# Performance work log

Measured on AMD Instinct MI355X. Metric: run time of the kernel, lower is better.

Reference implementation:

```python
import jax, jax.numpy as jnp
import numpy as np

B, P, T, V, H, E, C = 256, 256, 32, 3433, 512, 300, 128


def _gru(x, h, W_ih, W_hh, b_ih, b_hh):
    # torch.nn.GRUCell math (bias=True default)
    gx = x @ W_ih.T + b_ih          # (B, 3H)
    gh = h @ W_hh.T + b_hh          # (B, 3H)
    xr, xz, xn = jnp.split(gx, 3, axis=-1)
    hr, hz, hn = jnp.split(gh, 3, axis=-1)
    r = jax.nn.sigmoid(xr + hr)
    z = jax.nn.sigmoid(xz + hz)
    n = jnp.tanh(xn + r * hn)
    return (1.0 - z) * n + z * h


def setup_inputs() -> dict:
    key = jax.random.key(0)
    ks = jax.random.split(key, 24)
    s = 0.02
    inp = {
        'word_embs': jax.random.normal(ks[0], (B, T, E), jnp.float32),
        't_feat': jax.random.normal(ks[1], (B, C), jnp.float32),
        'c_feats': jax.random.normal(ks[2], (B, P, C), jnp.float32),
        'num_words': T,
        # top-down unit (all Linears bias=False)
        'W_td1': jax.random.normal(ks[3], (128, H), jnp.float32) * s,
        'W_td2': jax.random.normal(ks[4], (128, C), jnp.float32) * s,
        'W_td3': jax.random.normal(ks[5], (128, E), jnp.float32) * s,
        'W_td':  jax.random.normal(ks[6], (128, 128), jnp.float32) * s,
        'W1_ih': jax.random.normal(ks[7], (3 * H, 128), jnp.float32) * s,
        'W1_hh': jax.random.normal(ks[8], (3 * H, H), jnp.float32) * s,
        'b1_ih': jax.random.normal(ks[9], (3 * H,), jnp.float32) * s,
        'b1_hh': jax.random.normal(ks[10], (3 * H,), jnp.float32) * s,
        # additive attention
        'W_feat': jax.random.normal(ks[11], (H, C), jnp.float32) * s,
        'W_hidd': jax.random.normal(ks[12], (H, H), jnp.float32) * s,
        'W_att':  jax.random.normal(ks[13], (1, H), jnp.float32) * s,
        # language unit
        'W_l1': jax.random.normal(ks[14], (128, C), jnp.float32) * s,
        'W_l2': jax.random.normal(ks[15], (128, H), jnp.float32) * s,
        'W_l':  jax.random.normal(ks[16], (128, 128), jnp.float32) * s,
        'W2_ih': jax.random.normal(ks[17], (3 * H, 128), jnp.float32) * s,
        'W2_hh': jax.random.normal(ks[18], (3 * H, H), jnp.float32) * s,
        'b2_ih': jax.random.normal(ks[19], (3 * H,), jnp.float32) * s,
        'b2_hh': jax.random.normal(ks[20], (3 * H,), jnp.float32) * s,
        # classifier (bias=True)
        'W_cls': jax.random.normal(ks[21], (V, H), jnp.float32) * s,
        'b_cls': jax.random.normal(ks[22], (V,), jnp.float32) * s,
    }
    return inp


def reference(word_embs, t_feat, c_feats, num_words,
              W_td1, W_td2, W_td3, W_td, W1_ih, W1_hh, b1_ih, b1_hh,
              W_feat, W_hidd, W_att, W_l1, W_l2, W_l,
              W2_ih, W2_hh, b2_ih, b2_hh, W_cls, b_cls):
    n_steps = num_words - 1  # python int, static
    # precompute attention key projection of proposals: (B, P, H)
    feat_proj = jnp.einsum('bpc,hc->bph', c_feats, W_feat)
    td_t = t_feat @ W_td2.T  # (B, 128), time-invariant

    def step_fn(carry, x_t):
        h1, h2 = carry
        # top-down input
        s = x_t @ W_td3.T + h2 @ W_td1.T + td_t
        s = jax.nn.relu(jnp.tanh(s) @ W_td.T)
        h1 = _gru(s, h1, W1_ih, W1_hh, b1_ih, b1_hh)
        # additive attention over proposals
        comb = jnp.tanh(feat_proj + (h1 @ W_hidd.T)[:, None, :])  # (B, P, H)
        scores = jnp.einsum('bph,h->bp', comb, W_att[0])           # (B, P)
        mask = jax.nn.softmax(scores, axis=1)                      # (B, P)
        attended = jnp.einsum('bpc,bp->bc', c_feats, mask)         # (B, C)
        # language input
        l = jnp.tanh(attended @ W_l1.T + h1 @ W_l2.T)
        l = jax.nn.relu(l @ W_l.T)
        h2 = _gru(l, h2, W2_ih, W2_hh, b2_ih, b2_hh)
        logits = h2 @ W_cls.T + b_cls                              # (B, V)
        return (h1, h2), (logits, mask)

    h0 = (jnp.zeros((word_embs.shape[0], H), word_embs.dtype),
          jnp.zeros((word_embs.shape[0], H), word_embs.dtype))
    xs = jnp.swapaxes(word_embs[:, :n_steps], 0, 1)  # (T-1, B, E)
    _, (logits, masks) = jax.lax.scan(step_fn, h0, xs)
    lang_cap = jnp.swapaxes(logits, 0, 1)            # (B, T-1, V)
    topdown_attn = jnp.transpose(masks, (1, 2, 0))   # (B, P, T-1)
    return lang_cap, topdown_attn
```

## Files before the change

kernel.cpp:

```cpp
#include <hip/hip_runtime.h>
#include <hip/hip_bf16.h>

namespace {

constexpr int kB  = 256;
constexpr int kP  = 256;
constexpr int kT  = 32;
constexpr int kNS = 31;
constexpr int kV  = 3433;
constexpr int kH  = 512;
constexpr int kE  = 300;
constexpr int kC  = 128;
constexpr int kG  = 1536;
constexpr int kLdsStride = 40;

typedef __bf16 bf16x8 __attribute__((ext_vector_type(8)));
typedef float f32x4 __attribute__((ext_vector_type(4)));

__device__ __forceinline__ float fexp2(float x) {
  float r; asm("v_exp_f32 %0, %1" : "=v"(r) : "v"(x)); return r;
}
__device__ __forceinline__ float frcp(float x) {
  float r; asm("v_rcp_f32 %0, %1" : "=v"(r) : "v"(x)); return r;
}
__device__ __forceinline__ float ftanh(float x) {
  float e = fexp2(x * 2.8853900817779268f);
  return 1.0f - 2.0f * frcp(e + 1.0f);
}
__device__ __forceinline__ float fsigm(float x) {
  return frcp(1.0f + fexp2(x * -1.4426950408889634f));
}
__device__ __forceinline__ unsigned short f2bf(float f) {
  unsigned u = __float_as_uint(f);
  u += 0x7FFFu + ((u >> 16) & 1u);
  return (unsigned short)(u >> 16);
}
__device__ __forceinline__ float bf2f(unsigned short s) {
  return __uint_as_float((unsigned)s << 16);
}
__device__ __forceinline__ bf16x8 bload(const unsigned short* p) {
  union { uint4 u; bf16x8 v; } x;
  x.u = *(const uint4*)p;
  return x.v;
}

__global__ void k_transpose(const float* s0, const float* s1, const float* s2,
                            const float* s3, const float* s4, const float* s5,
                            const float* s6, const float* s7, const float* s8,
                            float* d0, float* d1, float* d2, float* d3,
                            float* d4, float* d5, float* d6, float* d7,
                            float* d8) {
  const float* src; float* dst; int R, Cd;
  switch (blockIdx.y) {
    case 0:  src = s0; dst = d0; R = 128;  Cd = 300; break;
    case 1:  src = s1; dst = d1; R = 128;  Cd = 512; break;
    case 2:  src = s2; dst = d2; R = 128;  Cd = 128; break;
    case 3:  src = s3; dst = d3; R = 128;  Cd = 128; break;
    case 4:  src = s4; dst = d4; R = 128;  Cd = 512; break;
    case 5:  src = s5; dst = d5; R = 128;  Cd = 128; break;
    case 6:  src = s6; dst = d6; R = 1536; Cd = 128; break;
    case 7:  src = s7; dst = d7; R = 1536; Cd = 128; break;
    default: src = s8; dst = d8; R = 512;  Cd = 512; break;
  }
  int n = R * Cd;
  for (int i = blockIdx.x * blockDim.x + threadIdx.x; i < n;
       i += gridDim.x * blockDim.x) {
    int k = i / R, r = i - k * R;
    dst[i] = src[r * Cd + k];
  }
}

__global__ void k_tobf16(const float* s0, const float* s1, const float* s2,
                         const float* s3, const float* s4, const float* s5,
                         const float* s6, const float* s7,
                         unsigned short* d0, unsigned short* d1,
                         unsigned short* d2, unsigned short* d3,
                         unsigned short* d4, unsigned short* d5,
                         unsigned short* d6, unsigned short* d7) {
  const float* s; unsigned short* d; int n;
  switch (blockIdx.y) {
    case 0:  s = s0; d = d0; n = kC * kC; break;
    case 1:  s = s1; d = d1; n = kH * kC; break;
    case 2:  s = s2; d = d2; n = kC * kC; break;
    case 3:  s = s3; d = d3; n = kC * kG; break;
    case 4:  s = s4; d = d4; n = kH * kH; break;
    case 5:  s = s5; d = d5; n = kH * kC; break;
    case 6:  s = s6; d = d6; n = kC * kC; break;
    default: s = s7; d = d7; n = kC * kG; break;
  }
  for (int i = blockIdx.x * blockDim.x + threadIdx.x; i < n;
       i += gridDim.x * blockDim.x)
    d[i] = f2bf(s[i]);
}

__global__ void k_split(const float* s0, const float* s1, const float* s2,
                        const float* s3,
                        unsigned short* h0, unsigned short* l0,
                        unsigned short* h1, unsigned short* l1,
                        unsigned short* h2, unsigned short* l2,
                        unsigned short* h3, unsigned short* l3) {
  const float* s; unsigned short* h; unsigned short* l; int n;
  switch (blockIdx.y) {
    case 0:  s = s0; h = h0; l = l0; n = kG * kH; break;
    case 1:  s = s1; h = h1; l = l1; n = kG * kH; break;
    case 2:  s = s2; h = h2; l = l2; n = kV * kH; break;
    default: s = s3; h = h3; l = l3; n = kH * kC; break;
  }
  for (int i = blockIdx.x * blockDim.x + threadIdx.x; i < n;
       i += gridDim.x * blockDim.x) {
    float v = s[i];
    unsigned short hb = f2bf(v);
    h[i] = hb;
    l[i] = f2bf(v - bf2f(hb));
  }
}

__global__ void k_init(const float* __restrict__ t_feat,
                       const float* __restrict__ W_td2,
                       float* __restrict__ td, float* __restrict__ h1,
                       float* __restrict__ h2,
                       unsigned short* __restrict__ h1h,
                       unsigned short* __restrict__ h1l,
                       unsigned short* __restrict__ h2h,
                       unsigned short* __restrict__ h2l) {
  int tid = blockIdx.x * 256 + threadIdx.x;
  int b = tid >> 7, c = tid & 127;
  const float* tf = t_feat + b * kC;
  const float* w  = W_td2 + c * kC;
  float acc = 0.f;
  for (int k = 0; k < kC; ++k) acc = fmaf(tf[k], w[k], acc);
  td[tid] = acc;
  for (int i = tid; i < kB * kH; i += (1 << 15)) {
    h1[i] = 0.f; h2[i] = 0.f;
    h1h[i] = 0; h1l[i] = 0; h2h[i] = 0; h2l[i] = 0;
  }
}

__global__ __launch_bounds__(256) void k_xw(
    const float* __restrict__ word_embs, const float* __restrict__ td3t,
    const float* __restrict__ td, float* __restrict__ xw) {
  __shared__ float xl[4 * 300];
  __shared__ float tdl[512];
  int t = blockIdx.y, b0 = blockIdx.x * 4, tid = threadIdx.x;
  #pragma unroll
  for (int r = 0; r < 4; ++r) {
    const float* xs = word_embs + (size_t)(b0 + r) * (kT * kE) + (size_t)t * kE;
    for (int e = tid; e < kE; e += 256) xl[r * kE + e] = xs[e];
  }
  for (int i = tid; i < 512; i += 256) tdl[i] = td[(size_t)b0 * kC + i];
  __syncthreads();
  #pragma unroll
  for (int q = 0; q < 2; ++q) {
    int idx = tid + q * 256;
    int r = idx >> 7, c = idx & 127;
    float acc = tdl[idx];
    const float* xr = xl + r * kE;
    const float* w3 = td3t + c;
    for (int e = 0; e < kE; ++e) acc = fmaf(xr[e], w3[(size_t)e * 128], acc);
    xw[((size_t)t * kB + b0 + r) * kC + c] = acc;
  }
}

__global__ __launch_bounds__(256) void k_prestep(
    const float* __restrict__ xw, const unsigned short* __restrict__ tdbt,
    const unsigned short* __restrict__ iht1b, const float* __restrict__ b1_ih,
    float* __restrict__ gx1) {
  __shared__ float s1l[128];
  __shared__ float s2l[128];
  __shared__ float part[256];
  int b = blockIdx.x, tid = threadIdx.x;
  if (tid < 128) s1l[tid] = ftanh(xw[(size_t)b * kC + tid]);
  __syncthreads();
  {
    int c = tid & 127, g = tid >> 7;
    float s = 0.f;
    const unsigned short* w = tdbt + (size_t)(g * 64) * kC + c;
    for (int k = 0; k < 64; ++k)
      s = fmaf(s1l[g * 64 + k], bf2f(w[(size_t)k * kC]), s);
    part[g * 128 + c] = s;
  }
  __syncthreads();
  if (tid < 128) s2l[tid] = fmaxf(part[tid] + part[128 + tid], 0.f);
  __syncthreads();
  #pragma unroll
  for (int q = 0; q < 6; ++q) {
    int j = q * 256 + tid;
    float acc = b1_ih[j];
    const unsigned short* w = iht1b + j;
    for (int k = 0; k < kC; ++k)
      acc = fmaf(s2l[k], bf2f(w[(size_t)k * kG]), acc);
    gx1[(size_t)b * kG + j] = acc;
  }
}

__device__ __forceinline__ void mm_tile_lds(
    const unsigned short* __restrict__ Ah, const unsigned short* __restrict__ Al,
    const unsigned short* __restrict__ Bh, const unsigned short* __restrict__ Bl,
    int m0, int n0, int K, int kbeg, int kend, int nMax, f32x4 acc[4][4],
    unsigned short* sAh, unsigned short* sAl,
    unsigned short* sBh, unsigned short* sBl) {
  int tid = threadIdx.x;
  int lane = tid & 63, wid = tid >> 6;
  int wm = (wid >> 1) * 64, wn = (wid & 1) * 64;
  int r16 = lane & 15, kq = lane >> 4;
  int rA = tid >> 2, cA = (tid & 3) * 8;
  int brow0 = n0 + rA;       if (brow0 > nMax) brow0 = nMax;
  int brow1 = n0 + rA + 64;  if (brow1 > nMax) brow1 = nMax;
  for (int k0 = kbeg; k0 < kend; k0 += 32) {
    uint4 va0 = *(const uint4*)(Ah + (size_t)(m0 + rA) * K + k0 + cA);
    uint4 va1 = *(const uint4*)(Ah + (size_t)(m0 + rA + 64) * K + k0 + cA);
    uint4 vb0 = *(const uint4*)(Al + (size_t)(m0 + rA) * K + k0 + cA);
    uint4 vb1 = *(const uint4*)(Al + (size_t)(m0 + rA + 64) * K + k0 + cA);
    uint4 vc0 = *(const uint4*)(Bh + (size_t)brow0 * K + k0 + cA);
    uint4 vc1 = *(const uint4*)(Bh + (size_t)brow1 * K + k0 + cA);
    uint4 vd0 = *(const uint4*)(Bl + (size_t)brow0 * K + k0 + cA);
    uint4 vd1 = *(const uint4*)(Bl + (size_t)brow1 * K + k0 + cA);
    __syncthreads();
    *(uint4*)&sAh[rA * kLdsStride + cA] = va0;
    *(uint4*)&sAh[(rA + 64) * kLdsStride + cA] = va1;
    *(uint4*)&sAl[rA * kLdsStride + cA] = vb0;
    *(uint4*)&sAl[(rA + 64) * kLdsStride + cA] = vb1;
    *(uint4*)&sBh[rA * kLdsStride + cA] = vc0;
    *(uint4*)&sBh[(rA + 64) * kLdsStride + cA] = vc1;
    *(uint4*)&sBl[rA * kLdsStride + cA] = vd0;
    *(uint4*)&sBl[(rA + 64) * kLdsStride + cA] = vd1;
    __syncthreads();
    bf16x8 ah[4], al[4], bh[4], bl[4];
    #pragma unroll
    for (int i = 0; i < 4; ++i) {
      int ar = (wm + i * 16 + r16) * kLdsStride + kq * 8;
      int br = (wn + i * 16 + r16) * kLdsStride + kq * 8;
      ah[i] = *(const bf16x8*)&sAh[ar];
      al[i] = *(const bf16x8*)&sAl[ar];
      bh[i] = *(const bf16x8*)&sBh[br];
      bl[i] = *(const bf16x8*)&sBl[br];
    }
    #pragma unroll
    for (int i = 0; i < 4; ++i)
      #pragma unroll
      for (int j = 0; j < 4; ++j) {
        acc[i][j] = __builtin_amdgcn_mfma_f32_16x16x32_bf16(ah[i], bh[j], acc[i][j], 0, 0, 0);
        acc[i][j] = __builtin_amdgcn_mfma_f32_16x16x32_bf16(ah[i], bl[j], acc[i][j], 0, 0, 0);
        acc[i][j] = __builtin_amdgcn_mfma_f32_16x16x32_bf16(al[i], bh[j], acc[i][j], 0, 0, 0);
      }
  }
}

__global__ __launch_bounds__(256) void k_featproj(
    const float* __restrict__ A, const unsigned short* __restrict__ Wh,
    const unsigned short* __restrict__ Wl, unsigned short* __restrict__ out) {
  int lane = threadIdx.x & 63, wid = threadIdx.x >> 6;
  int wm = (wid >> 1) * 64, wn = (wid & 1) * 64;
  int r16 = lane & 15, kq = lane >> 4;
  int m0 = blockIdx.x * 128, n0 = blockIdx.y * 128;
  f32x4 acc[4][4];
  #pragma unroll
  for (int i = 0; i < 4; ++i)
    #pragma unroll
    for (int j = 0; j < 4; ++j) acc[i][j] = (f32x4){0.f, 0.f, 0.f, 0.f};
  for (int k0 = 0; k0 < kC; k0 += 32) {
    int kk = k0 + kq * 8;
    bf16x8 ah[4], al[4], bh[4], bl[4];
    #pragma unroll
    for (int i = 0; i < 4; ++i) {
      const float* pa = A + (size_t)(m0 + wm + i * 16 + r16) * kC + kk;
      float4 v0 = *(const float4*)pa;
      float4 v1 = *(const float4*)(pa + 4);
      float vv[8] = {v0.x, v0.y, v0.z, v0.w, v1.x, v1.y, v1.z, v1.w};
      union { unsigned short s[8]; bf16x8 v; } uh, ul;
      #pragma unroll
      for (int q = 0; q < 8; ++q) {
        unsigned short hb = f2bf(vv[q]);
        uh.s[q] = hb;
        ul.s[q] = f2bf(vv[q] - bf2f(hb));
      }
      ah[i] = uh.v; al[i] = ul.v;
      const unsigned short* pb = Wh + (size_t)(n0 + wn + i * 16 + r16) * kC + kk;
      const unsigned short* pl = Wl + (size_t)(n0 + wn + i * 16 + r16) * kC + kk;
      bh[i] = bload(pb); bl[i] = bload(pl);
    }
    #pragma unroll
    for (int i = 0; i < 4; ++i)
      #pragma unroll
      for (int j = 0; j < 4; ++j) {
        acc[i][j] = __builtin_amdgcn_mfma_f32_16x16x32_bf16(ah[i], bh[j], acc[i][j], 0, 0, 0);
        acc[i][j] = __builtin_amdgcn_mfma_f32_16x16x32_bf16(ah[i], bl[j], acc[i][j], 0, 0, 0);
        acc[i][j] = __builtin_amdgcn_mfma_f32_16x16x32_bf16(al[i], bh[j], acc[i][j], 0, 0, 0);
      }
  }
  #pragma unroll
  for (int i = 0; i < 4; ++i)
    #pragma unroll
    for (int j = 0; j < 4; ++j)
      #pragma unroll
      for (int r = 0; r < 4; ++r) {
        int m = m0 + wm + i * 16 + kq * 4 + r;
        int n = n0 + wn + j * 16 + r16;
        out[(size_t)m * kH + n] = f2bf(acc[i][j][r]);
      }
}

__global__ __launch_bounds__(256) void k_gh(
    const unsigned short* __restrict__ h1h, const unsigned short* __restrict__ h1l,
    const unsigned short* __restrict__ h2h, const unsigned short* __restrict__ h2l,
    const unsigned short* __restrict__ w1hh_h, const unsigned short* __restrict__ w1hh_l,
    const unsigned short* __restrict__ w2hh_h, const unsigned short* __restrict__ w2hh_l,
    const float* __restrict__ b1_hh, const float* __restrict__ b2_hh,
    float* __restrict__ gh1, float* __restrict__ gh2) {
  __shared__ __align__(16) unsigned short sAh[128 * kLdsStride];
  __shared__ __align__(16) unsigned short sAl[128 * kLdsStride];
  __shared__ __align__(16) unsigned short sBh[128 * kLdsStride];
  __shared__ __align__(16) unsigned short sBl[128 * kLdsStride];
  int g2 = blockIdx.x;
  int half = g2 & 1, g = g2 >> 1;
  const unsigned short *Ah, *Al, *Wh, *Wl; const float* bias; float* out;
  if (g < 24) { Ah = h1h; Al = h1l; Wh = w1hh_h; Wl = w1hh_l;
                bias = b1_hh; out = gh1; }
  else { g -= 24; Ah = h2h; Al = h2l; Wh = w2hh_h; Wl = w2hh_l;
         bias = b2_hh; out = gh2; }
  out += (size_t)half * (kB * kG);
  int m0 = (g / 12) * 128, n0 = (g % 12) * 128;
  f32x4 acc[4][4];
  #pragma unroll
  for (int i = 0; i < 4; ++i)
    #pragma unroll
    for (int j = 0; j < 4; ++j) acc[i][j] = (f32x4){0.f, 0.f, 0.f, 0.f};
  mm_tile_lds(Ah, Al, Wh, Wl, m0, n0, kH, half * 256, half * 256 + 256,
              kG - 1, acc, sAh, sAl, sBh, sBl);
  int tid = threadIdx.x;
  int lane = tid & 63, wid = tid >> 6;
  int wm = (wid >> 1) * 64, wn = (wid & 1) * 64;
  int r16 = lane & 15, kq = lane >> 4;
  #pragma unroll
  for (int i = 0; i < 4; ++i)
    #pragma unroll
    for (int j = 0; j < 4; ++j)
      #pragma unroll
      for (int r = 0; r < 4; ++r) {
        int m = m0 + wm + i * 16 + kq * 4 + r;
        int n = n0 + wn + j * 16 + r16;
        float v = acc[i][j][r];
        if (half == 0) v += bias[n];
        out[(size_t)m * kG + n] = v;
      }
}

__global__ __launch_bounds__(1024, 4) void k_step2(
    float* __restrict__ gx1, const float* __restrict__ gh1,
    const float* __restrict__ gh2,
    float* __restrict__ h1, float* __restrict__ h2,
    unsigned short* __restrict__ h1h, unsigned short* __restrict__ h1l,
    unsigned short* __restrict__ h2h, unsigned short* __restrict__ h2l,
    const unsigned short* __restrict__ whdbT, const float* __restrict__ W_att,
    const unsigned short* __restrict__ fp, const float* __restrict__ c_feats,
    const unsigned short* __restrict__ l1bt, const unsigned short* __restrict__ l2bt,
    const unsigned short* __restrict__ lbt, const unsigned short* __restrict__ iht2b,
    const float* __restrict__ b2_ih,
    const unsigned short* __restrict__ td1bt, const unsigned short* __restrict__ tdbt,
    const unsigned short* __restrict__ iht1b, const float* __restrict__ b1_ih,
    const float* __restrict__ xw,
    unsigned short* __restrict__ h2all_h, unsigned short* __restrict__ h2all_l,
    float* __restrict__ mask_ws, int t) {
  __shared__ float partbuf[8192];
  __shared__ float h1p[512];
  __shared__ float h2p[512];
  __shared__ float hqs[512];
  __shared__ float scs[256];
  __shared__ float red[16];
  __shared__ float red2[16];
  __shared__ float attl[128];
  __shared__ float lt1[128];
  __shared__ float llv[128];
  __shared__ float s1l[128];
  __shared__ float s2l[128];
  __shared__ float gx2l[1536];
  const int b = blockIdx.x;
  const int tid = threadIdx.x;
  const int lane = tid & 63, wv = tid >> 6;
  const size_t GPART = (size_t)kB * kG;

  if (tid < 512) {
    int c = tid;
    float gr = gx1[(size_t)b * kG + c];
    float gz = gx1[(size_t)b * kG + 512 + c];
    float gn = gx1[(size_t)b * kG + 1024 + c];
    float hr = gh1[(size_t)b * kG + c] + gh1[GPART + (size_t)b * kG + c];
    float hz = gh1[(size_t)b * kG + 512 + c] + gh1[GPART + (size_t)b * kG + 512 + c];
    float hnv = gh1[(size_t)b * kG + 1024 + c] + gh1[GPART + (size_t)b * kG + 1024 + c];
    float rr = fsigm(gr + hr);
    float zz = fsigm(gz + hz);
    float nn = ftanh(gn + rr * hnv);
    float ho = h1[(size_t)b * kH + c];
    float hn = (1.f - zz) * nn + zz * ho;
    h1[(size_t)b * kH + c] = hn;
    h1p[c] = hn;
    unsigned short hb = f2bf(hn);
    h1h[(size_t)b * kH + c] = hb;
    h1l[(size_t)b * kH + c] = f2bf(hn - bf2f(hb));
  }
  __syncthreads();

  {
    int cg = tid & 63, kg = tid >> 6;
    int c0 = cg * 8;
    const unsigned short* w = whdbT + (size_t)(kg * 32) * kH + c0;
    float acc[8] = {};
    #pragma unroll 4
    for (int k = 0; k < 32; ++k) {
      union { uint4 u; unsigned short s[8]; } wu;
      wu.u = *(const uint4*)(w + (size_t)k * kH);
      float h = h1p[kg * 32 + k];
      #pragma unroll
      for (int j = 0; j < 8; ++j) acc[j] = fmaf(h, bf2f(wu.s[j]), acc[j]);
    }
    float* pp = &partbuf[kg * 512 + c0];
    #pragma unroll
    for (int j = 0; j < 8; ++j) pp[j] = acc[j];
  }
  __syncthreads();
  if (tid < 512) {
    float s = 0.f;
    #pragma unroll
    for (int g = 0; g < 16; ++g) s += partbuf[g * 512 + tid];
    hqs[tid] = s;
  }
  __syncthreads();

  {
    float hq8[8], aw[8];
    #pragma unroll
    for (int j = 0; j < 8; ++j) hq8[j] = hqs[lane * 8 + j];
    {
      float4 a0 = *(const float4*)(W_att + lane * 8);
      float4 a1 = *(const float4*)(W_att + lane * 8 + 4);
      aw[0] = a0.x; aw[1] = a0.y; aw[2] = a0.z; aw[3] = a0.w;
      aw[4] = a1.x; aw[5] = a1.y; aw[6] = a1.z; aw[7] = a1.w;
    }
    const unsigned short* fpb = fp + (size_t)b * kP * kH;
    int p0 = wv * 16;
    uint4 rv = *(const uint4*)(fpb + (size_t)p0 * kH + lane * 8);
    for (int p = p0; p < p0 + 16; ++p) {
      union { uint4 v; unsigned short s[8]; } u; u.v = rv;
      if (p + 1 < p0 + 16)
        rv = *(const uint4*)(fpb + (size_t)(p + 1) * kH + lane * 8);
      float sc = 0.f;
      #pragma unroll
      for (int j = 0; j < 8; ++j) {
        float f = __uint_as_float((unsigned)u.s[j] << 16);
        sc += aw[j] * ftanh(f + hq8[j]);
      }
      #pragma unroll
      for (int m = 32; m; m >>= 1) sc += __shfl_xor(sc, m, 64);
      if (lane == 0) scs[p] = sc;
    }
  }
  __syncthreads();

  {
    float sv = (tid < 256) ? scs[tid] : -1e30f;
    float mx = sv;
    #pragma unroll
    for (int m = 32; m; m >>= 1) mx = fmaxf(mx, __shfl_xor(mx, m, 64));
    if (lane == 0) red[wv] = mx;
    __syncthreads();
    float bm = red[0];
    #pragma unroll
    for (int i = 1; i < 16; ++i) bm = fmaxf(bm, red[i]);
    float ev = (tid < 256) ? fexp2((sv - bm) * 1.4426950408889634f) : 0.f;
    float sm = ev;
    #pragma unroll
    for (int m = 32; m; m >>= 1) sm += __shfl_xor(sm, m, 64);
    if (lane == 0) red2[wv] = sm;
    __syncthreads();
    float tot = 0.f;
    #pragma unroll
    for (int i = 0; i < 16; ++i) tot += red2[i];
    if (tid < 256) {
      float mk = ev * frcp(tot);
      scs[tid] = mk;
      mask_ws[(size_t)t * (kB * kP) + (size_t)b * kP + tid] = mk;
    }
  }
  __syncthreads();

  {
    int c = tid & 127, q = tid >> 7;
    const float* cf = c_feats + ((size_t)b * kP + q * 32) * kC + c;
    const float* ms = scs + q * 32;
    float acc = 0.f;
    for (int p = 0; p < 32; ++p) acc = fmaf(ms[p], cf[(size_t)p * kC], acc);
    partbuf[q * 128 + c] = acc;
  }
  __syncthreads();
  if (tid < 128) {
    float s = 0.f;
    #pragma unroll
    for (int q = 0; q < 8; ++q) s += partbuf[q * 128 + tid];
    attl[tid] = s;
  }
  __syncthreads();

  {
    if (tid < 512) {
      int cg = tid & 15, kg = tid >> 4;
      int c0 = cg * 8;
      const unsigned short* w = l2bt + (size_t)(kg * 16) * kC + c0;
      float acc[8] = {};
      for (int k = 0; k < 16; ++k) {
        union { uint4 u; unsigned short s[8]; } wu;
        wu.u = *(const uint4*)(w + (size_t)k * kC);
        float h = h1p[kg * 16 + k];
        #pragma unroll
        for (int j = 0; j < 8; ++j) acc[j] = fmaf(h, bf2f(wu.s[j]), acc[j]);
      }
      float* pp = &partbuf[kg * 128 + c0];
      #pragma unroll
      for (int j = 0; j < 8; ++j) pp[j] = acc[j];
    } else if (tid < 768) {
      int tt = tid - 512;
      int cg = tt & 15, kg = tt >> 4;
      int c0 = cg * 8;
      const unsigned short* w = l1bt + (size_t)(kg * 8) * kC + c0;
      float acc[8] = {};
      for (int k = 0; k < 8; ++k) {
        union { uint4 u; unsigned short s[8]; } wu;
        wu.u = *(const uint4*)(w + (size_t)k * kC);
        float a = attl[kg * 8 + k];
        #pragma unroll
        for (int j = 0; j < 8; ++j) acc[j] = fmaf(a, bf2f(wu.s[j]), acc[j]);
      }
      float* pp = &partbuf[4096 + kg * 128 + c0];
      #pragma unroll
      for (int j = 0; j < 8; ++j) pp[j] = acc[j];
    }
  }
  __syncthreads();
  if (tid < 128) {
    float s = 0.f;
    #pragma unroll
    for (int g = 0; g < 32; ++g) s += partbuf[g * 128 + tid];
    #pragma unroll
    for (int g = 0; g < 16; ++g) s += partbuf[4096 + g * 128 + tid];
    lt1[tid] = ftanh(s);
  }
  __syncthreads();

  if (tid < 256) {
    int cg = tid & 15, kg = tid >> 4;
    int c0 = cg * 8;
    const unsigned short* w = lbt + (size_t)(kg * 8) * kC + c0;
    float acc[8] = {};
    for (int k = 0; k < 8; ++k) {
      union { uint4 u; unsigned short s[8]; } wu;
      wu.u = *(const uint4*)(w + (size_t)k * kC);
      float l = lt1[kg * 8 + k];
      #pragma unroll
      for (int j = 0; j < 8; ++j) acc[j] = fmaf(l, bf2f(wu.s[j]), acc[j]);
    }
    float* pp = &partbuf[kg * 128 + c0];
    #pragma unroll
    for (int j = 0; j < 8; ++j) pp[j] = acc[j];
  }
  __syncthreads();
  if (tid < 128) {
    float s = 0.f;
    #pragma unroll
    for (int g = 0; g < 16; ++g) s += partbuf[g * 128 + tid];
    llv[tid] = fmaxf(s, 0.f);
  }
  __syncthreads();

  if (tid < 768) {
    int cg = tid % 192, kg = tid / 192;
    int c0 = cg * 8;
    const unsigned short* w = iht2b + (size_t)(kg * 32) * kG + c0;
    float acc[8] = {};
    #pragma unroll 4
    for (int k = 0; k < 32; ++k) {
      union { uint4 u; unsigned short s[8]; } wu;
      wu.u = *(const uint4*)(w + (size_t)k * kG);
      float l = llv[kg * 32 + k];
      #pragma unroll
      for (int j = 0; j < 8; ++j) acc[j] = fmaf(l, bf2f(wu.s[j]), acc[j]);
    }
    float* pp = &partbuf[kg * 1536 + c0];
    #pragma unroll
    for (int j = 0; j < 8; ++j) pp[j] = acc[j];
  }
  __syncthreads();
  for (int c = tid; c < kG; c += 1024) {
    float s = b2_ih[c];
    #pragma unroll
    for (int g = 0; g < 4; ++g) s += partbuf[g * 1536 + c];
    gx2l[c] = s;
  }
  __syncthreads();
  if (tid < 512) {
    int c = tid;
    float ghr = gh2[(size_t)b * kG + c] + gh2[GPART + (size_t)b * kG + c];
    float ghz = gh2[(size_t)b * kG + 512 + c] + gh2[GPART + (size_t)b * kG + 512 + c];
    float ghn = gh2[(size_t)b * kG + 1024 + c] + gh2[GPART + (size_t)b * kG + 1024 + c];
    float rr = fsigm(gx2l[c] + ghr);
    float zz = fsigm(gx2l[512 + c] + ghz);
    float nn = ftanh(gx2l[1024 + c] + rr * ghn);
    float ho = h2[(size_t)b * kH + c];
    float hn = (1.f - zz) * nn + zz * ho;
    h2[(size_t)b * kH + c] = hn;
    h2p[c] = hn;
    unsigned short hb = f2bf(hn);
    unsigned short lb = f2bf(hn - bf2f(hb));
    h2h[(size_t)b * kH + c] = hb;
    h2l[(size_t)b * kH + c] = lb;
    size_t o = ((size_t)t * kB + b) * kH + c;
    h2all_h[o] = hb;
    h2all_l[o] = lb;
  }
  __syncthreads();

  if (t + 1 < kNS) {
    if (tid < 512) {
      int cg = tid & 15, kg = tid >> 4;
      int c0 = cg * 8;
      const unsigned short* w = td1bt + (size_t)(kg * 16) * kC + c0;
      float acc[8] = {};
      for (int k = 0; k < 16; ++k) {
        union { uint4 u; unsigned short s[8]; } wu;
        wu.u = *(const uint4*)(w + (size_t)k * kC);
        float h = h2p[kg * 16 + k];
        #pragma unroll
        for (int j = 0; j < 8; ++j) acc[j] = fmaf(h, bf2f(wu.s[j]), acc[j]);
      }
      float* pp = &partbuf[kg * 128 + c0];
      #pragma unroll
      for (int j = 0; j < 8; ++j) pp[j] = acc[j];
    }
    __syncthreads();
    if (tid < 128) {
      float s = xw[((size_t)(t + 1) * kB + b) * kC + tid];
      #pragma unroll
      for (int g = 0; g < 32; ++g) s += partbuf[g * 128 + tid];
      s1l[tid] = ftanh(s);
    }
    __syncthreads();
    if (tid < 256) {
      int cg = tid & 15, kg = tid >> 4;
      int c0 = cg * 8;
      const unsigned short* w = tdbt + (size_t)(kg * 8) * kC + c0;
      float acc[8] = {};
      for (int k = 0; k < 8; ++k) {
        union { uint4 u; unsigned short s[8]; } wu;
        wu.u = *(const uint4*)(w + (size_t)k * kC);
        float sv = s1l[kg * 8 + k];
        #pragma unroll
        for (int j = 0; j < 8; ++j) acc[j] = fmaf(sv, bf2f(wu.s[j]), acc[j]);
      }
      float* pp = &partbuf[kg * 128 + c0];
      #pragma unroll
      for (int j = 0; j < 8; ++j) pp[j] = acc[j];
    }
    __syncthreads();
    if (tid < 128) {
      float s = 0.f;
      #pragma unroll
      for (int g = 0; g < 16; ++g) s += partbuf[g * 128 + tid];
      s2l[tid] = fmaxf(s, 0.f);
    }
    __syncthreads();
    if (tid < 768) {
      int cg = tid % 192, kg = tid / 192;
      int c0 = cg * 8;
      const unsigned short* w = iht1b + (size_t)(kg * 32) * kG + c0;
      float acc[8] = {};
      #pragma unroll 4
      for (int k = 0; k < 32; ++k) {
        union { uint4 u; unsigned short s[8]; } wu;
        wu.u = *(const uint4*)(w + (size_t)k * kG);
        float sv = s2l[kg * 32 + k];
        #pragma unroll
        for (int j = 0; j < 8; ++j) acc[j] = fmaf(sv, bf2f(wu.s[j]), acc[j]);
      }
      float* pp = &partbuf[kg * 1536 + c0];
      #pragma unroll
      for (int j = 0; j < 8; ++j) pp[j] = acc[j];
    }
    __syncthreads();
    for (int c = tid; c < kG; c += 1024) {
      float s = b1_ih[c];
      #pragma unroll
      for (int g = 0; g < 4; ++g) s += partbuf[g * 1536 + c];
      gx1[(size_t)b * kG + c] = s;
    }
  }
}

__global__ __launch_bounds__(256) void k_atrans(
    const float* __restrict__ mws, float* __restrict__ attn_out) {
  __shared__ float tile[256][33];
  int pair0 = blockIdx.x * 256;
  int tid = threadIdx.x;
  #pragma unroll
  for (int t = 0; t < kNS; ++t)
    tile[tid][t] = mws[(size_t)t * (kB * kP) + pair0 + tid];
  __syncthreads();
  float* outb = attn_out + (size_t)pair0 * kNS;
  #pragma unroll
  for (int i = 0; i < kNS; ++i) {
    int g = i * 256 + tid;
    int pr = g / 31, tt = g - pr * 31;
    outb[g] = tile[pr][tt];
  }
}

__global__ __launch_bounds__(256) void k_cls(
    const unsigned short* __restrict__ Ah, const unsigned short* __restrict__ Al,
    const unsigned short* __restrict__ Wh, const unsigned short* __restrict__ Wl,
    const float* __restrict__ bc, float* __restrict__ out) {
  __shared__ __align__(16) unsigned short sAh[128 * kLdsStride];
  __shared__ __align__(16) unsigned short sAl[128 * kLdsStride];
  __shared__ __align__(16) unsigned short sBh[128 * kLdsStride];
  __shared__ __align__(16) unsigned short sBl[128 * kLdsStride];
  int m0 = blockIdx.x * 128, n0 = blockIdx.y * 128;
  f32x4 acc[4][4];
  #pragma unroll
  for (int i = 0; i < 4; ++i)
    #pragma unroll
    for (int j = 0; j < 4; ++j) acc[i][j] = (f32x4){0.f, 0.f, 0.f, 0.f};
  mm_tile_lds(Ah, Al, Wh, Wl, m0, n0, kH, 0, kH, kV - 1, acc,
              sAh, sAl, sBh, sBl);
  int lane = threadIdx.x & 63, wid = threadIdx.x >> 6;
  int wm = (wid >> 1) * 64, wn = (wid & 1) * 64;
  int r16 = lane & 15, kq = lane >> 4;
  #pragma unroll
  for (int i = 0; i < 4; ++i)
    #pragma unroll
    for (int j = 0; j < 4; ++j)
      #pragma unroll
      for (int r = 0; r < 4; ++r) {
        int m = m0 + wm + i * 16 + kq * 4 + r;
        int n = n0 + wn + j * 16 + r16;
        if (n < kV) {
          int tt = m >> 8, b = m & 255;
          out[(size_t)b * (kNS * kV) + (size_t)tt * kV + n] = acc[i][j][r] + bc[n];
        }
      }
}

}

extern "C" void kernel_launch(void* const* d_in, const int* in_sizes, int n_in,
                              void* d_out, int out_size, void* d_ws,
                              size_t ws_size, hipStream_t stream) {
  (void)in_sizes; (void)n_in; (void)out_size; (void)ws_size;
  const float* word_embs = (const float*)d_in[0];
  const float* t_feat    = (const float*)d_in[1];
  const float* c_feats   = (const float*)d_in[2];
  const float* W_td1 = (const float*)d_in[4];
  const float* W_td2 = (const float*)d_in[5];
  const float* W_td3 = (const float*)d_in[6];
  const float* W_td  = (const float*)d_in[7];
  const float* W1_ih = (const float*)d_in[8];
  const float* W1_hh = (const float*)d_in[9];
  const float* b1_ih = (const float*)d_in[10];
  const float* b1_hh = (const float*)d_in[11];
  const float* W_feat = (const float*)d_in[12];
  const float* W_hidd = (const float*)d_in[13];
  const float* W_att  = (const float*)d_in[14];
  const float* W_l1 = (const float*)d_in[15];
  const float* W_l2 = (const float*)d_in[16];
  const float* W_l  = (const float*)d_in[17];
  const float* W2_ih = (const float*)d_in[18];
  const float* W2_hh = (const float*)d_in[19];
  const float* b2_ih = (const float*)d_in[20];
  const float* b2_hh = (const float*)d_in[21];
  const float* W_cls = (const float*)d_in[22];
  const float* b_cls = (const float*)d_in[23];

  float* lang = (float*)d_out;
  float* attn_out = lang + (size_t)kB * kNS * kV;
  unsigned short* fp = (unsigned short*)d_out;

  float* p = (float*)d_ws;
  float* h1 = p;      p += kB * kH;
  float* h2 = p;      p += kB * kH;
  float* td = p;      p += kB * kC;
  float* gx1 = p;     p += (size_t)kB * kG;
  float* gh1 = p;     p += (size_t)2 * kB * kG;
  float* gh2 = p;     p += (size_t)2 * kB * kG;
  float* mask_ws = p; p += (size_t)kNS * kB * kP;
  float* xw = p;      p += (size_t)kNS * kB * kC;
  float* td3t = p;    p += kE * 128;
  float* td1t = p;    p += kH * 128;
  float* tdt  = p;    p += 128 * 128;
  float* l1t  = p;    p += 128 * 128;
  float* l2t  = p;    p += kH * 128;
  float* lt   = p;    p += 128 * 128;
  float* iht1 = p;    p += 128 * kG;
  float* iht2 = p;    p += 128 * kG;
  float* whd_t = p;   p += kH * kH;

  unsigned short* u = (unsigned short*)p;
  unsigned short* h1h = u;     u += kB * kH;
  unsigned short* h1l = u;     u += kB * kH;
  unsigned short* h2h = u;     u += kB * kH;
  unsigned short* h2l = u;     u += kB * kH;
  unsigned short* w1hh_h = u;  u += (size_t)kG * kH;
  unsigned short* w1hh_l = u;  u += (size_t)kG * kH;
  unsigned short* w2hh_h = u;  u += (size_t)kG * kH;
  unsigned short* w2hh_l = u;  u += (size_t)kG * kH;
  unsigned short* wc_h = u;    u += (size_t)kV * kH;
  unsigned short* wc_l = u;    u += (size_t)kV * kH;
  unsigned short* wf_h = u;    u += (size_t)kH * kC;
  unsigned short* wf_l = u;    u += (size_t)kH * kC;
  unsigned short* h2all_h = u; u += (size_t)kNS * kB * kH;
  unsigned short* h2all_l = u; u += (size_t)kNS * kB * kH;
  unsigned short* l1bt = u;    u += kC * kC;
  unsigned short* l2bt = u;    u += (size_t)kH * kC;
  unsigned short* lbt = u;     u += kC * kC;
  unsigned short* iht2b = u;   u += (size_t)kC * kG;
  unsigned short* whdbT = u;   u += (size_t)kH * kH;
  unsigned short* td1bt = u;   u += (size_t)kH * kC;
  unsigned short* tdbt = u;    u += kC * kC;
  unsigned short* iht1b = u;   u += (size_t)kC * kG;

  k_transpose<<<dim3(64, 9), 256, 0, stream>>>(
      W_td3, W_td1, W_td, W_l1, W_l2, W_l, W1_ih, W2_ih, W_hidd,
      td3t, td1t, tdt, l1t, l2t, lt, iht1, iht2, whd_t);
  k_tobf16<<<dim3(96, 8), 256, 0, stream>>>(
      l1t, l2t, lt, iht2, whd_t, td1t, tdt, iht1,
      l1bt, l2bt, lbt, iht2b, whdbT, td1bt, tdbt, iht1b);
  k_split<<<dim3(256, 4), 256, 0, stream>>>(
      W1_hh, W2_hh, W_cls, W_feat,
      w1hh_h, w1hh_l, w2hh_h, w2hh_l, wc_h, wc_l, wf_h, wf_l);
  k_init<<<128, 256, 0, stream>>>(t_feat, W_td2, td, h1, h2,
                                  h1h, h1l, h2h, h2l);
  k_featproj<<<dim3(512, 4), 256, 0, stream>>>(c_feats, wf_h, wf_l, fp);
  k_xw<<<dim3(64, kNS), 256, 0, stream>>>(word_embs, td3t, td, xw);
  k_prestep<<<256, 256, 0, stream>>>(xw, tdbt, iht1b, b1_ih, gx1);

  for (int t = 0; t < kNS; ++t) {
    k_gh<<<96, 256, 0, stream>>>(h1h, h1l, h2h, h2l,
                                 w1hh_h, w1hh_l, w2hh_h, w2hh_l,
                                 b1_hh, b2_hh, gh1, gh2);
    k_step2<<<256, 1024, 0, stream>>>(gx1, gh1, gh2, h1, h2,
                                      h1h, h1l, h2h, h2l, whdbT, W_att, fp,
                                      c_feats, l1bt, l2bt, lbt, iht2b, b2_ih,
                                      td1bt, tdbt, iht1b, b1_ih, xw,
                                      h2all_h, h2all_l, mask_ws, t);
  }
  k_atrans<<<256, 256, 0, stream>>>(mask_ws, attn_out);
  k_cls<<<dim3(62, 27), 256, 0, stream>>>(h2all_h, h2all_l, wc_h, wc_l,
                                          b_cls, lang);
}
```

Measured before the change: 2.226 ms.

## Move top-down gx1 precompute into gh kernel and swizzle LDS layout

The per-step top-down input chain (h2·W_td1, tanh, W_td, relu, W1_ih) now runs in 64 extra blocks of the renamed k_pre kernel, alongside the recurrent gh matmul blocks. Previously it ran serially at the tail of each k_step2 block, and the separate k_prestep launch is removed. The shared-memory matmul tiles also switch from a padded stride of 40 to an unpadded stride of 32 with an XOR swizzle, which cuts LDS use and is meant to avoid bank conflicts. The gx1 work now processes 4 batch rows per block with fewer threads, which may be slower per block but is taken off the k_step2 critical path.

```diff
diff --git a/kernel.cpp b/kernel.cpp
--- a/kernel.cpp
+++ b/kernel.cpp
@@ -12,7 +12,6 @@
 constexpr int kE  = 300;
 constexpr int kC  = 128;
 constexpr int kG  = 1536;
-constexpr int kLdsStride = 40;
 
 typedef __bf16 bf16x8 __attribute__((ext_vector_type(8)));
 typedef float f32x4 __attribute__((ext_vector_type(4)));
@@ -37,11 +36,6 @@
 }
 __device__ __forceinline__ float bf2f(unsigned short s) {
   return __uint_as_float((unsigned)s << 16);
-}
-__device__ __forceinline__ bf16x8 bload(const unsigned short* p) {
-  union { uint4 u; bf16x8 v; } x;
-  x.u = *(const uint4*)p;
-  return x.v;
 }
 
 __global__ void k_transpose(const float* s0, const float* s1, const float* s2,
@@ -161,38 +155,6 @@
   }
 }
 
-__global__ __launch_bounds__(256) void k_prestep(
-    const float* __restrict__ xw, const unsigned short* __restrict__ tdbt,
-    const unsigned short* __restrict__ iht1b, const float* __restrict__ b1_ih,
-    float* __restrict__ gx1) {
-  __shared__ float s1l[128];
-  __shared__ float s2l[128];
-  __shared__ float part[256];
-  int b = blockIdx.x, tid = threadIdx.x;
-  if (tid < 128) s1l[tid] = ftanh(xw[(size_t)b * kC + tid]);
-  __syncthreads();
-  {
-    int c = tid & 127, g = tid >> 7;
-    float s = 0.f;
-    const unsigned short* w = tdbt + (size_t)(g * 64) * kC + c;
-    for (int k = 0; k < 64; ++k)
-      s = fmaf(s1l[g * 64 + k], bf2f(w[(size_t)k * kC]), s);
-    part[g * 128 + c] = s;
-  }
-  __syncthreads();
-  if (tid < 128) s2l[tid] = fmaxf(part[tid] + part[128 + tid], 0.f);
-  __syncthreads();
-  #pragma unroll
-  for (int q = 0; q < 6; ++q) {
-    int j = q * 256 + tid;
-    float acc = b1_ih[j];
-    const unsigned short* w = iht1b + j;
-    for (int k = 0; k < kC; ++k)
-      acc = fmaf(s2l[k], bf2f(w[(size_t)k * kG]), acc);
-    gx1[(size_t)b * kG + j] = acc;
-  }
-}
-
 __device__ __forceinline__ void mm_tile_lds(
     const unsigned short* __restrict__ Ah, const unsigned short* __restrict__ Al,
     const unsigned short* __restrict__ Bh, const unsigned short* __restrict__ Bl,
@@ -203,7 +165,10 @@
   int lane = tid & 63, wid = tid >> 6;
   int wm = (wid >> 1) * 64, wn = (wid & 1) * 64;
   int r16 = lane & 15, kq = lane >> 4;
-  int rA = tid >> 2, cA = (tid & 3) * 8;
+  int rA = tid >> 2;
+  int swSlot = (((tid & 3) ^ ((rA >> 1) & 3)) * 8);
+  int cA = (tid & 3) * 8;
+  int swr = (kq ^ ((r16 >> 1) & 3)) * 8;
   int brow0 = n0 + rA;       if (brow0 > nMax) brow0 = nMax;
   int brow1 = n0 + rA + 64;  if (brow1 > nMax) brow1 = nMax;
   for (int k0 = kbeg; k0 < kend; k0 += 32) {
@@ -216,20 +181,20 @@
     uint4 vd0 = *(const uint4*)(Bl + (size_t)brow0 * K + k0 + cA);
     uint4 vd1 = *(const uint4*)(Bl + (size_t)brow1 * K + k0 + cA);
     __syncthreads();
-    *(uint4*)&sAh[rA * kLdsStride + cA] = va0;
-    *(uint4*)&sAh[(rA + 64) * kLdsStride + cA] = va1;
-    *(uint4*)&sAl[rA * kLdsStride + cA] = vb0;
-    *(uint4*)&sAl[(rA + 64) * kLdsStride + cA] = vb1;
-    *(uint4*)&sBh[rA * kLdsStride + cA] = vc0;
-    *(uint4*)&sBh[(rA + 64) * kLdsStride + cA] = vc1;
-    *(uint4*)&sBl[rA * kLdsStride + cA] = vd0;
-    *(uint4*)&sBl[(rA + 64) * kLdsStride + cA] = vd1;
+    *(uint4*)&sAh[rA * 32 + swSlot] = va0;
+    *(uint4*)&sAh[(rA + 64) * 32 + swSlot] = va1;
+    *(uint4*)&sAl[rA * 32 + swSlot] = vb0;
+    *(uint4*)&sAl[(rA + 64) * 32 + swSlot] = vb1;
+    *(uint4*)&sBh[rA * 32 + swSlot] = vc0;
+    *(uint4*)&sBh[(rA + 64) * 32 + swSlot] = vc1;
+    *(uint4*)&sBl[rA * 32 + swSlot] = vd0;
+    *(uint4*)&sBl[(rA + 64) * 32 + swSlot] = vd1;
     __syncthreads();
     bf16x8 ah[4], al[4], bh[4], bl[4];
     #pragma unroll
     for (int i = 0; i < 4; ++i) {
-      int ar = (wm + i * 16 + r16) * kLdsStride + kq * 8;
-      int br = (wn + i * 16 + r16) * kLdsStride + kq * 8;
+      int ar = (wm + i * 16 + r16) * 32 + swr;
+      int br = (wn + i * 16 + r16) * 32 + swr;
       ah[i] = *(const bf16x8*)&sAh[ar];
       al[i] = *(const bf16x8*)&sAl[ar];
       bh[i] = *(const bf16x8*)&sBh[br];
@@ -277,7 +242,9 @@
       ah[i] = uh.v; al[i] = ul.v;
       const unsigned short* pb = Wh + (size_t)(n0 + wn + i * 16 + r16) * kC + kk;
       const unsigned short* pl = Wl + (size_t)(n0 + wn + i * 16 + r16) * kC + kk;
-      bh[i] = bload(pb); bl[i] = bload(pl);
+      union { uint4 u; bf16x8 v; } xb, xl2;
+      xb.u = *(const uint4*)pb; xl2.u = *(const uint4*)pl;
+      bh[i] = xb.v; bl[i] = xl2.v;
     }
     #pragma unroll
     for (int i = 0; i < 4; ++i)
@@ -300,53 +267,152 @@
       }
 }
 
-__global__ __launch_bounds__(256) void k_gh(
+__global__ __launch_bounds__(256) void k_pre(
     const unsigned short* __restrict__ h1h, const unsigned short* __restrict__ h1l,
     const unsigned short* __restrict__ h2h, const unsigned short* __restrict__ h2l,
     const unsigned short* __restrict__ w1hh_h, const unsigned short* __restrict__ w1hh_l,
     const unsigned short* __restrict__ w2hh_h, const unsigned short* __restrict__ w2hh_l,
     const float* __restrict__ b1_hh, const float* __restrict__ b2_hh,
-    float* __restrict__ gh1, float* __restrict__ gh2) {
-  __shared__ __align__(16) unsigned short sAh[128 * kLdsStride];
-  __shared__ __align__(16) unsigned short sAl[128 * kLdsStride];
-  __shared__ __align__(16) unsigned short sBh[128 * kLdsStride];
-  __shared__ __align__(16) unsigned short sBl[128 * kLdsStride];
-  int g2 = blockIdx.x;
-  int half = g2 & 1, g = g2 >> 1;
-  const unsigned short *Ah, *Al, *Wh, *Wl; const float* bias; float* out;
-  if (g < 24) { Ah = h1h; Al = h1l; Wh = w1hh_h; Wl = w1hh_l;
-                bias = b1_hh; out = gh1; }
-  else { g -= 24; Ah = h2h; Al = h2l; Wh = w2hh_h; Wl = w2hh_l;
-         bias = b2_hh; out = gh2; }
-  out += (size_t)half * (kB * kG);
-  int m0 = (g / 12) * 128, n0 = (g % 12) * 128;
-  f32x4 acc[4][4];
-  #pragma unroll
-  for (int i = 0; i < 4; ++i)
-    #pragma unroll
-    for (int j = 0; j < 4; ++j) acc[i][j] = (f32x4){0.f, 0.f, 0.f, 0.f};
-  mm_tile_lds(Ah, Al, Wh, Wl, m0, n0, kH, half * 256, half * 256 + 256,
-              kG - 1, acc, sAh, sAl, sBh, sBl);
-  int tid = threadIdx.x;
-  int lane = tid & 63, wid = tid >> 6;
-  int wm = (wid >> 1) * 64, wn = (wid & 1) * 64;
-  int r16 = lane & 15, kq = lane >> 4;
-  #pragma unroll
-  for (int i = 0; i < 4; ++i)
-    #pragma unroll
-    for (int j = 0; j < 4; ++j)
+    float* __restrict__ gh1, float* __restrict__ gh2,
+    const float* __restrict__ h2, const float* __restrict__ xw, int t,
+    const unsigned short* __restrict__ td1bt, const unsigned short* __restrict__ tdbt,
+    const unsigned short* __restrict__ iht1b, const float* __restrict__ b1_ih,
+    float* __restrict__ gx1) {
+  __shared__ __align__(16) unsigned char smemraw[32768];
+  int blk = blockIdx.x, tid = threadIdx.x;
+  if (blk < 96) {
+    unsigned short* sAh = (unsigned short*)smemraw;
+    unsigned short* sAl = sAh + 4096;
+    unsigned short* sBh = sAl + 4096;
+    unsigned short* sBl = sBh + 4096;
+    int half = blk & 1, g = blk >> 1;
+    const unsigned short *Ah, *Al, *Wh, *Wl; const float* bias; float* out;
+    if (g < 24) { Ah = h1h; Al = h1l; Wh = w1hh_h; Wl = w1hh_l;
+                  bias = b1_hh; out = gh1; }
+    else { g -= 24; Ah = h2h; Al = h2l; Wh = w2hh_h; Wl = w2hh_l;
+           bias = b2_hh; out = gh2; }
+    out += (size_t)half * (kB * kG);
+    int m0 = (g / 12) * 128, n0 = (g % 12) * 128;
+    f32x4 acc[4][4];
+    #pragma unroll
+    for (int i = 0; i < 4; ++i)
+      #pragma unroll
+      for (int j = 0; j < 4; ++j) acc[i][j] = (f32x4){0.f, 0.f, 0.f, 0.f};
+    mm_tile_lds(Ah, Al, Wh, Wl, m0, n0, kH, half * 256, half * 256 + 256,
+                kG - 1, acc, sAh, sAl, sBh, sBl);
+    int lane = tid & 63, wid = tid >> 6;
+    int wm = (wid >> 1) * 64, wn = (wid & 1) * 64;
+    int r16 = lane & 15, kq = lane >> 4;
+    #pragma unroll
+    for (int i = 0; i < 4; ++i)
+      #pragma unroll
+      for (int j = 0; j < 4; ++j)
+        #pragma unroll
+        for (int r = 0; r < 4; ++r) {
+          int m = m0 + wm + i * 16 + kq * 4 + r;
+          int n = n0 + wn + j * 16 + r16;
+          float v = acc[i][j][r];
+          if (half == 0) v += bias[n];
+          out[(size_t)m * kG + n] = v;
+        }
+  } else {
+    float* h2loc = (float*)smemraw;
+    float* part  = h2loc + 2048;
+    float* s1    = part + 4096;
+    float* s2    = s1 + 512;
+    int b0 = (blk - 96) * 4;
+    for (int i = tid; i < 512; i += 256)
+      *(float4*)&h2loc[i * 4] = *(const float4*)(h2 + (size_t)b0 * kH + i * 4);
+    __syncthreads();
+    {
+      int cg = tid & 31, kg = tid >> 5;
+      float acc[4][4] = {};
+      for (int k = 0; k < 64; ++k) {
+        int gk = kg * 64 + k;
+        union { uint2 u; unsigned short s[4]; } wu;
+        wu.u = *(const uint2*)(td1bt + (size_t)gk * kC + cg * 4);
+        #pragma unroll
+        for (int r = 0; r < 4; ++r) {
+          float h = h2loc[r * 512 + gk];
+          acc[r][0] = fmaf(h, bf2f(wu.s[0]), acc[r][0]);
+          acc[r][1] = fmaf(h, bf2f(wu.s[1]), acc[r][1]);
+          acc[r][2] = fmaf(h, bf2f(wu.s[2]), acc[r][2]);
+          acc[r][3] = fmaf(h, bf2f(wu.s[3]), acc[r][3]);
+        }
+      }
+      #pragma unroll
+      for (int r = 0; r < 4; ++r)
+        #pragma unroll
+        for (int j = 0; j < 4; ++j)
+          part[kg * 512 + r * 128 + cg * 4 + j] = acc[r][j];
+    }
+    __syncthreads();
+    for (int idx = tid; idx < 512; idx += 256) {
+      int r = idx >> 7, c = idx & 127;
+      float s = xw[((size_t)t * kB + b0 + r) * kC + c];
+      #pragma unroll
+      for (int g = 0; g < 8; ++g) s += part[g * 512 + idx];
+      s1[idx] = ftanh(s);
+    }
+    __syncthreads();
+    {
+      int cg = tid & 31, kg = tid >> 5;
+      float acc[4][4] = {};
+      for (int k = 0; k < 16; ++k) {
+        int gk = kg * 16 + k;
+        union { uint2 u; unsigned short s[4]; } wu;
+        wu.u = *(const uint2*)(tdbt + (size_t)gk * kC + cg * 4);
+        #pragma unroll
+        for (int r = 0; r < 4; ++r) {
+          float h = s1[r * 128 + gk];
+          acc[r][0] = fmaf(h, bf2f(wu.s[0]), acc[r][0]);
+          acc[r][1] = fmaf(h, bf2f(wu.s[1]), acc[r][1]);
+          acc[r][2] = fmaf(h, bf2f(wu.s[2]), acc[r][2]);
+          acc[r][3] = fmaf(h, bf2f(wu.s[3]), acc[r][3]);
+        }
+      }
+      #pragma unroll
+      for (int r = 0; r < 4; ++r)
+        #pragma unroll
+        for (int j = 0; j < 4; ++j)
+          part[kg * 512 + r * 128 + cg * 4 + j] = acc[r][j];
+    }
+    __syncthreads();
+    for (int idx = tid; idx < 512; idx += 256) {
+      float s = 0.f;
+      #pragma unroll
+      for (int g = 0; g < 8; ++g) s += part[g * 512 + idx];
+      s2[idx] = fmaxf(s, 0.f);
+    }
+    __syncthreads();
+    for (int g = tid; g < 384; g += 256) {
+      int c0 = g * 4;
+      float acc[4][4] = {};
+      for (int k = 0; k < kC; ++k) {
+        union { uint2 u; unsigned short s[4]; } wu;
+        wu.u = *(const uint2*)(iht1b + (size_t)k * kG + c0);
+        #pragma unroll
+        for (int r = 0; r < 4; ++r) {
+          float h = s2[r * 128 + k];
+          acc[r][0] = fmaf(h, bf2f(wu.s[0]), acc[r][0]);
+          acc[r][1] = fmaf(h, bf2f(wu.s[1]), acc[r][1]);
+          acc[r][2] = fmaf(h, bf2f(wu.s[2]), acc[r][2]);
+          acc[r][3] = fmaf(h, bf2f(wu.s[3]), acc[r][3]);
+        }
+      }
+      float4 bv = *(const float4*)(b1_ih + c0);
       #pragma unroll
       for (int r = 0; r < 4; ++r) {
-        int m = m0 + wm + i * 16 + kq * 4 + r;
-        int n = n0 + wn + j * 16 + r16;
-        float v = acc[i][j][r];
-        if (half == 0) v += bias[n];
-        out[(size_t)m * kG + n] = v;
-      }
+        float4 o = make_float4(acc[r][0] + bv.x, acc[r][1] + bv.y,
+                               acc[r][2] + bv.z, acc[r][3] + bv.w);
+        *(float4*)(gx1 + (size_t)(b0 + r) * kG + c0) = o;
+      }
+    }
+  }
 }
 
 __global__ __launch_bounds__(1024, 4) void k_step2(
-    float* __restrict__ gx1, const float* __restrict__ gh1,
+    const float* __restrict__ gx1, const float* __restrict__ gh1,
     const float* __restrict__ gh2,
     float* __restrict__ h1, float* __restrict__ h2,
     unsigned short* __restrict__ h1h, unsigned short* __restrict__ h1l,
@@ -356,14 +422,10 @@
     const unsigned short* __restrict__ l1bt, const unsigned short* __restrict__ l2bt,
     const unsigned short* __restrict__ lbt, const unsigned short* __restrict__ iht2b,
     const float* __restrict__ b2_ih,
-    const unsigned short* __restrict__ td1bt, const unsigned short* __restrict__ tdbt,
-    const unsigned short* __restrict__ iht1b, const float* __restrict__ b1_ih,
-    const float* __restrict__ xw,
     unsigned short* __restrict__ h2all_h, unsigned short* __restrict__ h2all_l,
     float* __restrict__ mask_ws, int t) {
   __shared__ float partbuf[8192];
   __shared__ float h1p[512];
-  __shared__ float h2p[512];
   __shared__ float hqs[512];
   __shared__ float scs[256];
   __shared__ float red[16];
@@ -371,8 +433,6 @@
   __shared__ float attl[128];
   __shared__ float lt1[128];
   __shared__ float llv[128];
-  __shared__ float s1l[128];
-  __shared__ float s2l[128];
   __shared__ float gx2l[1536];
   const int b = blockIdx.x;
   const int tid = threadIdx.x;
@@ -606,7 +666,6 @@
     float ho = h2[(size_t)b * kH + c];
     float hn = (1.f - zz) * nn + zz * ho;
     h2[(size_t)b * kH + c] = hn;
-    h2p[c] = hn;
     unsigned short hb = f2bf(hn);
     unsigned short lb = f2bf(hn - bf2f(hb));
     h2h[(size_t)b * kH + c] = hb;
@@ -614,82 +673,6 @@
     size_t o = ((size_t)t * kB + b) * kH + c;
     h2all_h[o] = hb;
     h2all_l[o] = lb;
-  }
-  __syncthreads();
-
-  if (t + 1 < kNS) {
-    if (tid < 512) {
-      int cg = tid & 15, kg = tid >> 4;
-      int c0 = cg * 8;
-      const unsigned short* w = td1bt + (size_t)(kg * 16) * kC + c0;
-      float acc[8] = {};
-      for (int k = 0; k < 16; ++k) {
-        union { uint4 u; unsigned short s[8]; } wu;
-        wu.u = *(const uint4*)(w + (size_t)k * kC);
-        float h = h2p[kg * 16 + k];
-        #pragma unroll
-        for (int j = 0; j < 8; ++j) acc[j] = fmaf(h, bf2f(wu.s[j]), acc[j]);
-      }
-      float* pp = &partbuf[kg * 128 + c0];
-      #pragma unroll
-      for (int j = 0; j < 8; ++j) pp[j] = acc[j];
-    }
-    __syncthreads();
-    if (tid < 128) {
-      float s = xw[((size_t)(t + 1) * kB + b) * kC + tid];
-      #pragma unroll
-      for (int g = 0; g < 32; ++g) s += partbuf[g * 128 + tid];
-      s1l[tid] = ftanh(s);
-    }
-    __syncthreads();
-    if (tid < 256) {
-      int cg = tid & 15, kg = tid >> 4;
-      int c0 = cg * 8;
-      const unsigned short* w = tdbt + (size_t)(kg * 8) * kC + c0;
-      float acc[8] = {};
-      for (int k = 0; k < 8; ++k) {
-        union { uint4 u; unsigned short s[8]; } wu;
-        wu.u = *(const uint4*)(w + (size_t)k * kC);
-        float sv = s1l[kg * 8 + k];
-        #pragma unroll
-        for (int j = 0; j < 8; ++j) acc[j] = fmaf(sv, bf2f(wu.s[j]), acc[j]);
-      }
-      float* pp = &partbuf[kg * 128 + c0];
-      #pragma unroll
-      for (int j = 0; j < 8; ++j) pp[j] = acc[j];
-    }
-    __syncthreads();
-    if (tid < 128) {
-      float s = 0.f;
-      #pragma unroll
-      for (int g = 0; g < 16; ++g) s += partbuf[g * 128 + tid];
-      s2l[tid] = fmaxf(s, 0.f);
-    }
-    __syncthreads();
-    if (tid < 768) {
-      int cg = tid % 192, kg = tid / 192;
-      int c0 = cg * 8;
-      const unsigned short* w = iht1b + (size_t)(kg * 32) * kG + c0;
-      float acc[8] = {};
-      #pragma unroll 4
-      for (int k = 0; k < 32; ++k) {
-        union { uint4 u; unsigned short s[8]; } wu;
-        wu.u = *(const uint4*)(w + (size_t)k * kG);
-        float sv = s2l[kg * 32 + k];
-        #pragma unroll
-        for (int j = 0; j < 8; ++j) acc[j] = fmaf(sv, bf2f(wu.s[j]), acc[j]);
-      }
-      float* pp = &partbuf[kg * 1536 + c0];
-      #pragma unroll
-      for (int j = 0; j < 8; ++j) pp[j] = acc[j];
-    }
-    __syncthreads();
-    for (int c = tid; c < kG; c += 1024) {
-      float s = b1_ih[c];
-      #pragma unroll
-      for (int g = 0; g < 4; ++g) s += partbuf[g * 1536 + c];
-      gx1[(size_t)b * kG + c] = s;
-    }
   }
 }
 
@@ -715,10 +698,7 @@
     const unsigned short* __restrict__ Ah, const unsigned short* __restrict__ Al,
     const unsigned short* __restrict__ Wh, const unsigned short* __restrict__ Wl,
     const float* __restrict__ bc, float* __restrict__ out) {
-  __shared__ __align__(16) unsigned short sAh[128 * kLdsStride];
-  __shared__ __align__(16) unsigned short sAl[128 * kLdsStride];
-  __shared__ __align__(16) unsigned short sBh[128 * kLdsStride];
-  __shared__ __align__(16) unsigned short sBl[128 * kLdsStride];
+  __shared__ __align__(16) unsigned short sAh[4096], sAl[4096], sBh[4096], sBl[4096];
   int m0 = blockIdx.x * 128, n0 = blockIdx.y * 128;
   f32x4 acc[4][4];
   #pragma unroll
@@ -835,16 +815,15 @@
                                   h1h, h1l, h2h, h2l);
   k_featproj<<<dim3(512, 4), 256, 0, stream>>>(c_feats, wf_h, wf_l, fp);
   k_xw<<<dim3(64, kNS), 256, 0, stream>>>(word_embs, td3t, td, xw);
-  k_prestep<<<256, 256, 0, stream>>>(xw, tdbt, iht1b, b1_ih, gx1);
 
   for (int t = 0; t < kNS; ++t) {
-    k_gh<<<96, 256, 0, stream>>>(h1h, h1l, h2h, h2l,
-                                 w1hh_h, w1hh_l, w2hh_h, w2hh_l,
-                                 b1_hh, b2_hh, gh1, gh2);
+    k_pre<<<160, 256, 0, stream>>>(h1h, h1l, h2h, h2l,
+                                   w1hh_h, w1hh_l, w2hh_h, w2hh_l,
+                                   b1_hh, b2_hh, gh1, gh2,
+                                   h2, xw, t, td1bt, tdbt, iht1b, b1_ih, gx1);
     k_step2<<<256, 1024, 0, stream>>>(gx1, gh1, gh2, h1, h2,
                                       h1h, h1l, h2h, h2l, whdbT, W_att, fp,
                                       c_feats, l1bt, l2bt, lbt, iht2b, b2_ih,
-                                      td1bt, tdbt, iht1b, b1_ih, xw,
                                       h2all_h, h2all_l, mask_ws, t);
   }
   k_atrans<<<256, 256, 0, stream>>>(mask_ws, attn_out);
```

New measurement: 2.459 ms. 1.1x slower.
